# Kernel tuning notes

Measured on AMD Instinct MI355X. Metric: run time of the kernel, lower is better.

The kernel has to match this reference:

```python
import jax, jax.numpy as jnp
import numpy as np

L = 4      # number of layers (graph nodes)
B = 128    # batch
H = 4096   # neurons per layer


def setup_inputs() -> dict:
    key = jax.random.key(0)
    k1, k2, k3 = jax.random.split(key, 3)
    # per-layer source activations, stacked: [L, B, H]
    states = jax.random.normal(k1, (L, B, H), dtype=jnp.float32)
    # all Connection weight matrices, W[t, s] maps source s -> target t: [L, L, H_out, H_in]
    # scaled by 1/sqrt(H) so summed matmuls stay O(1) (original uses constant w_init)
    W = jax.random.normal(k2, (L, L, H, H), dtype=jnp.float32) * (1.0 / np.sqrt(H))
    # external inputs added into each target's current: [L, B, H]
    ext = jax.random.normal(k3, (L, B, H), dtype=jnp.float32)
    return {"states": states, "W": W, "ext": ext}


def reference(states, W, ext):
    # Synapses/Links: for each target t, sum over sources s of (x_s @ W[t,s].T)
    # (Connection.forward is x @ w.T). Single fused einsum replaces the
    # jit.fork fan-out over L*L small matmuls + Python-level sum.
    currents = jnp.einsum('sbh,tsoh->tbo', states, W) + ext  # [L, B, H]
    # Layer/Neurons: per-node activation function
    return jnp.tanh(currents)
```

## Files before the change

### kernel.cpp

```cpp
#include <hip/hip_runtime.h>
#include <hip/hip_bf16.h>
#include <stdint.h>

#define L_ 4
#define B_ 128
#define H_ 4096
#define BK 64
#define BN 32
#define KIT 256
#define NTHR 256
#define NTOT (L_*B_*H_)
#define WBYTES (BN*BK*2)

typedef _Float16 f16x8 __attribute__((ext_vector_type(8)));
typedef float    f32x4 __attribute__((ext_vector_type(4)));
typedef float    f4    __attribute__((ext_vector_type(4)));
typedef uint32_t u32x4 __attribute__((ext_vector_type(4)));
typedef uint32_t u32x2 __attribute__((ext_vector_type(2)));

__device__ __forceinline__ uint32_t pack2(float a, float b) {
  const _Float16 ha = (_Float16)a;
  const _Float16 hb = (_Float16)b;
  const uint32_t ua = (uint32_t)__builtin_bit_cast(uint16_t, ha);
  const uint32_t ub = (uint32_t)__builtin_bit_cast(uint16_t, hb);
  return ua | (ub << 16);
}

__global__ __launch_bounds__(NTHR)
void cvt_tile_kernel(const float* __restrict__ x, u32x4* __restrict__ ws)
{
  const int d   = blockIdx.x * NTHR + threadIdx.x;
  const int row = d & 127;
  const int lh  = (d >> 7) & 3;
  const int kk  = (d >> 9) & 1;
  const int kt  = d >> 10;
  const int s   = kt >> 6;
  const int kb  = kt & 63;
  const float* src = x + ((size_t)(s * B_ + row)) * H_ + kb * 64 + kk * 32 + lh * 8;
  f4 lo = *reinterpret_cast<const f4*>(src);
  f4 hi = *reinterpret_cast<const f4*>(src + 4);
  u32x4 v;
  v.x = pack2(lo.x, lo.y); v.y = pack2(lo.z, lo.w);
  v.z = pack2(hi.x, hi.y); v.w = pack2(hi.z, hi.w);
  ws[d] = v;
}

__device__ __forceinline__ void bar_lgkm0() {
  __builtin_amdgcn_sched_barrier(0);
  asm volatile("s_waitcnt lgkmcnt(0)");
  __builtin_amdgcn_sched_barrier(0);
  __builtin_amdgcn_s_barrier();
  __builtin_amdgcn_sched_barrier(0);
}

__global__ __launch_bounds__(NTHR, 2)
void net_gemm_kernel(const uint8_t* __restrict__ atiled,
                     const float* __restrict__ Wm,
                     const float* __restrict__ ext,
                     float* __restrict__ out)
{
  __shared__ __align__(16) uint8_t lds[2 * WBYTES];

  const int tid  = threadIdx.x;
  const int bid  = blockIdx.x;
  const int t    = bid >> 7;
  const int n0   = (bid & 127) * BN;

  const int wv   = tid >> 6;
  const int lane = tid & 63;
  const int lid  = lane & 15;
  const int lh   = lane >> 4;

  const uint8_t* a_base = atiled + lh * 2048 + (wv * 32 + lid) * 16;

  const int wrow = tid >> 4;
  const int wcol = (tid & 15) * 4;
  const float* w_base = Wm + ((size_t)t * L_ * H_ + (size_t)(n0 + wrow)) * H_ + wcol;
  const uint32_t w_st0 =
      (uint32_t)wrow * 128 + (((uint32_t)(tid & 15) * 8) ^ ((uint32_t)(wrow & 7) << 4));
  const uint32_t w_st1 = w_st0 + 16 * 128;

  uint32_t b_rd[2][2];
  #pragma unroll
  for (int nf = 0; nf < 2; ++nf)
    #pragma unroll
    for (int kk = 0; kk < 2; ++kk) {
      const int row = nf * 16 + lid;
      b_rd[nf][kk] = (uint32_t)row * 128 +
                     (((uint32_t)(kk * 64 + lh * 16)) ^ ((uint32_t)(lid & 7) << 4));
    }

  f32x4 acc[2][2] = {};

  f16x8 aS0[2][2], aS1[2][2], aS2[2][2];
  f4    wf0[2], wf1[2];

  auto LOADA = [&](int kt, f16x8 (&a)[2][2]) {
    const uint8_t* p = a_base + (size_t)kt * 16384;
    a[0][0] = *reinterpret_cast<const f16x8*>(p);
    a[1][0] = *reinterpret_cast<const f16x8*>(p + 256);
    a[0][1] = *reinterpret_cast<const f16x8*>(p + 8192);
    a[1][1] = *reinterpret_cast<const f16x8*>(p + 8192 + 256);
  };

  auto LOADW = [&](int kidx, f4 (&w)[2]) {
    const int s  = kidx >> 6;
    const int h0 = (kidx & 63) << 6;
    const float* wp = w_base + (size_t)s * ((size_t)H_ * H_) + h0;
    w[0] = __builtin_nontemporal_load(reinterpret_cast<const f4*>(wp));
    w[1] = __builtin_nontemporal_load(reinterpret_cast<const f4*>(wp + 16 * (size_t)H_));
  };

  auto WRITEW = [&](uint8_t* base, f4 (&w)[2]) {
    u32x2 w0, w1;
    w0.x = pack2(w[0].x, w[0].y); w0.y = pack2(w[0].z, w[0].w);
    w1.x = pack2(w[1].x, w[1].y); w1.y = pack2(w[1].z, w[1].w);
    *reinterpret_cast<u32x2*>(base + w_st0) = w0;
    *reinterpret_cast<u32x2*>(base + w_st1) = w1;
  };

  auto COMPUTE = [&](const uint8_t* base, f16x8 (&av)[2][2]) {
    f16x8 bv[2][2];
    #pragma unroll
    for (int nf = 0; nf < 2; ++nf)
      #pragma unroll
      for (int kk = 0; kk < 2; ++kk)
        bv[nf][kk] = *reinterpret_cast<const f16x8*>(base + b_rd[nf][kk]);
    #pragma unroll
    for (int kk = 0; kk < 2; ++kk)
      #pragma unroll
      for (int mf = 0; mf < 2; ++mf)
        #pragma unroll
        for (int nf = 0; nf < 2; ++nf)
          acc[mf][nf] = __builtin_amdgcn_mfma_f32_16x16x32_f16(
              av[mf][kk], bv[nf][kk], acc[mf][nf], 0, 0, 0);
  };

  uint8_t* buf0 = lds;
  uint8_t* buf1 = lds + WBYTES;

  LOADW(0, wf0);
  LOADW(1, wf1);
  LOADA(0, aS0);
  LOADA(1, aS1);
  WRITEW(buf0, wf0);
  bar_lgkm0();

  #define BODY(j_, AL_, AU_, WL_, WW_, BU_, BW_) do { \
      LOADA((j_) + 2, AL_);                           \
      LOADW((j_) + 2, WL_);                           \
      COMPUTE(BU_, AU_);                              \
      WRITEW(BW_, WW_);                               \
      bar_lgkm0();                                    \
    } while (0)

  #pragma unroll 1
  for (int k = 0; k < 252; k += 6) {
    BODY(k + 0, aS2, aS0, wf0, wf1, buf0, buf1);
    BODY(k + 1, aS0, aS1, wf1, wf0, buf1, buf0);
    BODY(k + 2, aS1, aS2, wf0, wf1, buf0, buf1);
    BODY(k + 3, aS2, aS0, wf1, wf0, buf1, buf0);
    BODY(k + 4, aS0, aS1, wf0, wf1, buf0, buf1);
    BODY(k + 5, aS1, aS2, wf1, wf0, buf1, buf0);
  }
  BODY(252, aS2, aS0, wf0, wf1, buf0, buf1);
  BODY(253, aS0, aS1, wf1, wf0, buf1, buf0);
  COMPUTE(buf0, aS2);
  WRITEW(buf1, wf1);
  bar_lgkm0();
  COMPUTE(buf1, aS0);
  #undef BODY

  #pragma unroll
  for (int mf = 0; mf < 2; ++mf)
    #pragma unroll
    for (int nf = 0; nf < 2; ++nf)
      #pragma unroll
      for (int j = 0; j < 4; ++j) {
        const int brow = wv * 32 + mf * 16 + lh * 4 + j;
        const int ocol = n0 + nf * 16 + lid;
        const size_t idx = ((size_t)(t * B_ + brow)) * H_ + ocol;
        out[idx] = tanhf(acc[mf][nf][j] + ext[idx]);
      }
}

#define FB_ABYTES (128*BK*2)
#define FB_BUFB   (FB_ABYTES+WBYTES)
__global__ __launch_bounds__(NTHR, 2)
void net_gemm_fb(const float* __restrict__ statesf,
                 const float* __restrict__ Wm,
                 const float* __restrict__ ext,
                 float* __restrict__ out)
{
  __shared__ __align__(16) uint8_t lds[2 * FB_BUFB];

  const int tid  = threadIdx.x;
  const int bid  = blockIdx.x;
  const int t    = bid >> 7;
  const int n0   = (bid & 127) * BN;
  const int wv   = tid >> 6;
  const int lane = tid & 63;
  const int lid  = lane & 15;
  const int lh   = lane >> 4;

  const int arow = tid >> 3;
  const int acol = (tid & 7) * 8;
  const uint32_t a_st_off =
      (uint32_t)arow * 128 + (((uint32_t)(tid & 7) * 16) ^ ((uint32_t)(arow & 7) << 4));
  const float* af_base = statesf + (size_t)arow * H_ + acol;

  const int wrow = tid >> 4;
  const int wcol = (tid & 15) * 4;
  const float* w_base = Wm + ((size_t)t * L_ * H_ + (size_t)(n0 + wrow)) * H_ + wcol;
  const uint32_t w_st0 =
      (uint32_t)FB_ABYTES + (uint32_t)wrow * 128 + (((uint32_t)(tid & 15) * 8) ^ ((uint32_t)(wrow & 7) << 4));
  const uint32_t w_st1 = w_st0 + 16 * 128;

  uint32_t a_rd[2][2], b_rd[2][2];
  #pragma unroll
  for (int mf = 0; mf < 2; ++mf)
    #pragma unroll
    for (int kk = 0; kk < 2; ++kk) {
      const int row = wv * 32 + mf * 16 + lid;
      a_rd[mf][kk] = (uint32_t)row * 128 +
                     (((uint32_t)(kk * 64 + lh * 16)) ^ ((uint32_t)(lid & 7) << 4));
    }
  #pragma unroll
  for (int nf = 0; nf < 2; ++nf)
    #pragma unroll
    for (int kk = 0; kk < 2; ++kk) {
      const int row = nf * 16 + lid;
      b_rd[nf][kk] = (uint32_t)FB_ABYTES + (uint32_t)row * 128 +
                     (((uint32_t)(kk * 64 + lh * 16)) ^ ((uint32_t)(lid & 7) << 4));
    }

  f32x4 acc[2][2] = {};
  f4 af0[4][2], af1[4][2], wf0[2], wf1[2];

  auto LOADg = [&](int kidx, f4 (&af)[4][2], f4 (&wfx)[2]) {
    const int s  = kidx >> 6;
    const int h0 = (kidx & 63) << 6;
    const float* ap = af_base + (size_t)s * (B_ * H_) + h0;
    #pragma unroll
    for (int j = 0; j < 4; ++j) {
      af[j][0] = *reinterpret_cast<const f4*>(ap + (size_t)j * (32 * H_));
      af[j][1] = *reinterpret_cast<const f4*>(ap + (size_t)j * (32 * H_) + 4);
    }
    const float* wp = w_base + (size_t)s * ((size_t)H_ * H_) + h0;
    wfx[0] = __builtin_nontemporal_load(reinterpret_cast<const f4*>(wp));
    wfx[1] = __builtin_nontemporal_load(reinterpret_cast<const f4*>(wp + 16 * (size_t)H_));
  };

  auto WRITEg = [&](uint8_t* base, f4 (&af)[4][2], f4 (&wfx)[2]) {
    #pragma unroll
    for (int j = 0; j < 4; ++j) {
      u32x4 v;
      v.x = pack2(af[j][0].x, af[j][0].y);
      v.y = pack2(af[j][0].z, af[j][0].w);
      v.z = pack2(af[j][1].x, af[j][1].y);
      v.w = pack2(af[j][1].z, af[j][1].w);
      *reinterpret_cast<u32x4*>(base + j * 4096 + a_st_off) = v;
    }
    u32x2 w0, w1;
    w0.x = pack2(wfx[0].x, wfx[0].y); w0.y = pack2(wfx[0].z, wfx[0].w);
    w1.x = pack2(wfx[1].x, wfx[1].y); w1.y = pack2(wfx[1].z, wfx[1].w);
    *reinterpret_cast<u32x2*>(base + w_st0) = w0;
    *reinterpret_cast<u32x2*>(base + w_st1) = w1;
  };

  auto COMPUTE = [&](const uint8_t* base) {
    f16x8 av[2][2], bv[2][2];
    #pragma unroll
    for (int mf = 0; mf < 2; ++mf)
      #pragma unroll
      for (int kk = 0; kk < 2; ++kk)
        av[mf][kk] = *reinterpret_cast<const f16x8*>(base + a_rd[mf][kk]);
    #pragma unroll
    for (int nf = 0; nf < 2; ++nf)
      #pragma unroll
      for (int kk = 0; kk < 2; ++kk)
        bv[nf][kk] = *reinterpret_cast<const f16x8*>(base + b_rd[nf][kk]);
    #pragma unroll
    for (int kk = 0; kk < 2; ++kk)
      #pragma unroll
      for (int mf = 0; mf < 2; ++mf)
        #pragma unroll
        for (int nf = 0; nf < 2; ++nf)
          acc[mf][nf] = __builtin_amdgcn_mfma_f32_16x16x32_f16(
              av[mf][kk], bv[nf][kk], acc[mf][nf], 0, 0, 0);
  };

  uint8_t* buf0 = lds;
  uint8_t* buf1 = lds + FB_BUFB;

  LOADg(0, af0, wf0);
  LOADg(1, af1, wf1);
  WRITEg(buf0, af0, wf0);
  bar_lgkm0();

  #pragma unroll 1
  for (int k = 0; k < 256; k += 2) {
    if (k + 2 < 256) LOADg(k + 2, af0, wf0);
    COMPUTE(buf0);
    WRITEg(buf1, af1, wf1);
    bar_lgkm0();
    if (k + 3 < 256) LOADg(k + 3, af1, wf1);
    COMPUTE(buf1);
    if (k + 2 < 256) {
      WRITEg(buf0, af0, wf0);
      bar_lgkm0();
    }
  }

  #pragma unroll
  for (int mf = 0; mf < 2; ++mf)
    #pragma unroll
    for (int nf = 0; nf < 2; ++nf)
      #pragma unroll
      for (int j = 0; j < 4; ++j) {
        const int brow = wv * 32 + mf * 16 + lh * 4 + j;
        const int ocol = n0 + nf * 16 + lid;
        const size_t idx = ((size_t)(t * B_ + brow)) * H_ + ocol;
        out[idx] = tanhf(acc[mf][nf][j] + ext[idx]);
      }
}

extern "C" void kernel_launch(void* const* d_in, const int* in_sizes, int n_in,
                              void* d_out, int out_size, void* d_ws, size_t ws_size,
                              hipStream_t stream) {
  const float* states = (const float*)d_in[0];
  const float* W      = (const float*)d_in[1];
  const float* ext    = (const float*)d_in[2];
  float* out          = (float*)d_out;

  const size_t st_bytes = (size_t)NTOT * 2;
  if (ws_size >= st_bytes) {
    const int nunits = NTOT / 8;
    cvt_tile_kernel<<<nunits / NTHR, NTHR, 0, stream>>>(states, (u32x4*)d_ws);
    net_gemm_kernel<<<512, NTHR, 0, stream>>>(
        (const uint8_t*)d_ws, W, ext, out);
  } else {
    net_gemm_fb<<<512, NTHR, 0, stream>>>(states, W, ext, out);
  }
}
```

Baseline: 242.8 us.

## Stage W in 256-wide K chunks with four sub-steps per barrier

Raises the W staging tile in the main GEMM kernel from 64 to 256 K-elements per LDS buffer. Each wave now loads 8 rows of 1KB contiguous W per stage instead of short strided pieces. Each barrier now covers four MFMA sub-steps, which should cut barrier and LDS sync overhead by about 4x and improve the global load pattern for the fp32 W stream. The cost is more registers held in flight for W (16 f4 vectors), a larger LDS footprint (32KB), and a shallower A prefetch, which could reduce occupancy or expose latency.

```diff
diff --git a/kernel.cpp b/kernel.cpp
--- a/kernel.cpp
+++ b/kernel.cpp
@@ -5,12 +5,12 @@
 #define L_ 4
 #define B_ 128
 #define H_ 4096
-#define BK 64
 #define BN 32
-#define KIT 256
+#define BKF 256
+#define SUP 64
 #define NTHR 256
 #define NTOT (L_*B_*H_)
-#define WBYTES (BN*BK*2)
+#define WTB (BN*BKF*2)
 
 typedef _Float16 f16x8 __attribute__((ext_vector_type(8)));
 typedef float    f32x4 __attribute__((ext_vector_type(4)));
@@ -59,7 +59,7 @@
                      const float* __restrict__ ext,
                      float* __restrict__ out)
 {
-  __shared__ __align__(16) uint8_t lds[2 * WBYTES];
+  __shared__ __align__(16) uint8_t lds[2 * WTB];
 
   const int tid  = threadIdx.x;
   const int bid  = blockIdx.x;
@@ -73,27 +73,41 @@
 
   const uint8_t* a_base = atiled + lh * 2048 + (wv * 32 + lid) * 16;
 
-  const int wrow = tid >> 4;
-  const int wcol = (tid & 15) * 4;
-  const float* w_base = Wm + ((size_t)t * L_ * H_ + (size_t)(n0 + wrow)) * H_ + wcol;
-  const uint32_t w_st0 =
-      (uint32_t)wrow * 128 + (((uint32_t)(tid & 15) * 8) ^ ((uint32_t)(wrow & 7) << 4));
-  const uint32_t w_st1 = w_st0 + 16 * 128;
+  const float* wp0 = Wm + (((size_t)t * L_) * H_ + (size_t)(n0 + wv * 8)) * H_ + lane * 4;
 
   uint32_t b_rd[2][2];
   #pragma unroll
   for (int nf = 0; nf < 2; ++nf)
     #pragma unroll
     for (int kk = 0; kk < 2; ++kk) {
-      const int row = nf * 16 + lid;
-      b_rd[nf][kk] = (uint32_t)row * 128 +
-                     (((uint32_t)(kk * 64 + lh * 16)) ^ ((uint32_t)(lid & 7) << 4));
+      const uint32_t row = (uint32_t)(nf * 16 + lid);
+      b_rd[nf][kk] = row * 512 +
+                     (((uint32_t)(kk * 64 + lh * 16)) ^ (((uint32_t)lid & 7) << 4));
     }
 
   f32x4 acc[2][2] = {};
 
-  f16x8 aS0[2][2], aS1[2][2], aS2[2][2];
-  f4    wf0[2], wf1[2];
+  f4    wRA[8], wRB[8];
+  f16x8 aA[2][2], aB[2][2];
+
+  auto LOADW = [&](int j, f4 (&w)[8]) {
+    const float* p = wp0 + (size_t)(j >> 4) * ((size_t)H_ * H_) + ((j & 15) << 8);
+    #pragma unroll
+    for (int i = 0; i < 8; ++i)
+      w[i] = __builtin_nontemporal_load(reinterpret_cast<const f4*>(p + (size_t)i * H_));
+  };
+
+  auto WRITEW = [&](uint8_t* base, f4 (&w)[8]) {
+    #pragma unroll
+    for (int i = 0; i < 8; ++i) {
+      u32x2 v;
+      v.x = pack2(w[i].x, w[i].y);
+      v.y = pack2(w[i].z, w[i].w);
+      const uint32_t off = (uint32_t)wv * 4096 + (uint32_t)i * 512 +
+                           (((uint32_t)lane * 8) ^ ((uint32_t)i << 4));
+      *reinterpret_cast<u32x2*>(base + off) = v;
+    }
+  };
 
   auto LOADA = [&](int kt, f16x8 (&a)[2][2]) {
     const uint8_t* p = a_base + (size_t)kt * 16384;
@@ -103,29 +117,13 @@
     a[1][1] = *reinterpret_cast<const f16x8*>(p + 8192 + 256);
   };
 
-  auto LOADW = [&](int kidx, f4 (&w)[2]) {
-    const int s  = kidx >> 6;
-    const int h0 = (kidx & 63) << 6;
-    const float* wp = w_base + (size_t)s * ((size_t)H_ * H_) + h0;
-    w[0] = __builtin_nontemporal_load(reinterpret_cast<const f4*>(wp));
-    w[1] = __builtin_nontemporal_load(reinterpret_cast<const f4*>(wp + 16 * (size_t)H_));
-  };
-
-  auto WRITEW = [&](uint8_t* base, f4 (&w)[2]) {
-    u32x2 w0, w1;
-    w0.x = pack2(w[0].x, w[0].y); w0.y = pack2(w[0].z, w[0].w);
-    w1.x = pack2(w[1].x, w[1].y); w1.y = pack2(w[1].z, w[1].w);
-    *reinterpret_cast<u32x2*>(base + w_st0) = w0;
-    *reinterpret_cast<u32x2*>(base + w_st1) = w1;
-  };
-
-  auto COMPUTE = [&](const uint8_t* base, f16x8 (&av)[2][2]) {
+  auto SUB = [&](const uint8_t* base, int skoff, f16x8 (&av)[2][2]) {
     f16x8 bv[2][2];
     #pragma unroll
     for (int nf = 0; nf < 2; ++nf)
       #pragma unroll
       for (int kk = 0; kk < 2; ++kk)
-        bv[nf][kk] = *reinterpret_cast<const f16x8*>(base + b_rd[nf][kk]);
+        bv[nf][kk] = *reinterpret_cast<const f16x8*>(base + b_rd[nf][kk] + skoff);
     #pragma unroll
     for (int kk = 0; kk < 2; ++kk)
       #pragma unroll
@@ -137,38 +135,39 @@
   };
 
   uint8_t* buf0 = lds;
-  uint8_t* buf1 = lds + WBYTES;
-
-  LOADW(0, wf0);
-  LOADW(1, wf1);
-  LOADA(0, aS0);
-  LOADA(1, aS1);
-  WRITEW(buf0, wf0);
+  uint8_t* buf1 = lds + WTB;
+
+  LOADW(0, wRA);
+  LOADW(1, wRB);
+  LOADA(0, aA);
+  WRITEW(buf0, wRA);
   bar_lgkm0();
 
-  #define BODY(j_, AL_, AU_, WL_, WW_, BU_, BW_) do { \
-      LOADA((j_) + 2, AL_);                           \
-      LOADW((j_) + 2, WL_);                           \
-      COMPUTE(BU_, AU_);                              \
-      WRITEW(BW_, WW_);                               \
-      bar_lgkm0();                                    \
+  #define BODY(j_, WLD_, WWT_, BUFC_, BUFW_) do {  \
+      LOADW((j_) + 2, WLD_);                       \
+      LOADA(4*(j_) + 1, aB); SUB(BUFC_, 0,   aA);  \
+      LOADA(4*(j_) + 2, aA); SUB(BUFC_, 128, aB);  \
+      LOADA(4*(j_) + 3, aB); SUB(BUFC_, 256, aA);  \
+      LOADA(4*(j_) + 4, aA); SUB(BUFC_, 384, aB);  \
+      WRITEW(BUFW_, WWT_);                         \
+      bar_lgkm0();                                 \
     } while (0)
 
   #pragma unroll 1
-  for (int k = 0; k < 252; k += 6) {
-    BODY(k + 0, aS2, aS0, wf0, wf1, buf0, buf1);
-    BODY(k + 1, aS0, aS1, wf1, wf0, buf1, buf0);
-    BODY(k + 2, aS1, aS2, wf0, wf1, buf0, buf1);
-    BODY(k + 3, aS2, aS0, wf1, wf0, buf1, buf0);
-    BODY(k + 4, aS0, aS1, wf0, wf1, buf0, buf1);
-    BODY(k + 5, aS1, aS2, wf1, wf0, buf1, buf0);
+  for (int j = 0; j < 62; j += 2) {
+    BODY(j,     wRA, wRB, buf0, buf1);
+    BODY(j + 1, wRB, wRA, buf1, buf0);
   }
-  BODY(252, aS2, aS0, wf0, wf1, buf0, buf1);
-  BODY(253, aS0, aS1, wf1, wf0, buf1, buf0);
-  COMPUTE(buf0, aS2);
-  WRITEW(buf1, wf1);
+  LOADA(249, aB); SUB(buf0, 0,   aA);
+  LOADA(250, aA); SUB(buf0, 128, aB);
+  LOADA(251, aB); SUB(buf0, 256, aA);
+  LOADA(252, aA); SUB(buf0, 384, aB);
+  WRITEW(buf1, wRB);
   bar_lgkm0();
-  COMPUTE(buf1, aS0);
+  LOADA(253, aB); SUB(buf1, 0,   aA);
+  LOADA(254, aA); SUB(buf1, 128, aB);
+  LOADA(255, aB); SUB(buf1, 256, aA);
+                  SUB(buf1, 384, aB);
   #undef BODY
 
   #pragma unroll
@@ -184,8 +183,10 @@
       }
 }
 
-#define FB_ABYTES (128*BK*2)
-#define FB_BUFB   (FB_ABYTES+WBYTES)
+#define FBK 64
+#define FB_ABYTES (128*FBK*2)
+#define FB_WBYTES (BN*FBK*2)
+#define FB_BUFB   (FB_ABYTES+FB_WBYTES)
 __global__ __launch_bounds__(NTHR, 2)
 void net_gemm_fb(const float* __restrict__ statesf,
                  const float* __restrict__ Wm,
```

Measured after the change: 217.3 us. 10.5% less time.
